# Performance work log

Measured on AMD Instinct MI355X. Metric: run time of the kernel, lower is better.

Reference implementation:

```python
import jax, jax.numpy as jnp
from jax import lax
import numpy as np

DECAY = 0.5   # LIF membrane leak factor
VTH = 1.0     # firing threshold


def _conv(x, w, stride, pad):
    # x: [B,C,H,W], w: [O,I,kh,kw]
    return lax.conv_general_dilated(
        x, w, (stride, stride), [(pad, pad), (pad, pad)],
        dimension_numbers=('NCHW', 'OIHW', 'NCHW'))


def _convT(x, w, b, stride=2, pad=1):
    # torch ConvTranspose2d(in,out,k,stride,pad): w is [Cin,Cout,k,k]
    k = w.shape[-1]
    wf = jnp.flip(w, (-2, -1)).transpose(1, 0, 2, 3)  # -> [Cout,Cin,k,k]
    y = lax.conv_general_dilated(
        x, wf, (1, 1), [(k - 1 - pad, k - 1 - pad)] * 2,
        lhs_dilation=(stride, stride),
        dimension_numbers=('NCHW', 'OIHW', 'NCHW'))
    return y + b[None, :, None, None]


def setup_inputs() -> dict:
    key = jax.random.key(0)
    ks = jax.random.split(key, 8)
    T, B = 16, 32
    x_seq = (jax.random.uniform(ks[0], (T, B, 1, 100, 368)) < 0.1).astype(jnp.float32)

    def p(k, shape, fan_in):
        return jax.random.normal(k, shape, jnp.float32) * (1.0 / np.sqrt(fan_in))

    return {
        'x_seq': x_seq,
        'w1': p(ks[1], (16, 1, 5, 5), 25),
        'w2': p(ks[2], (32, 16, 3, 3), 16 * 9),
        'wd': p(ks[3], (64, 32, 3, 3), 32 * 9),
        'bd': jnp.zeros((64,), jnp.float32),
        'wt1': p(ks[4], (64, 32, 4, 4), 64 * 16),
        'bt1': jnp.zeros((32,), jnp.float32),
        'wt2': p(ks[5], (32, 2, 4, 4), 32 * 16),
        'bt2': jnp.zeros((2,), jnp.float32),
        'actual_batch_size': 32,
    }


def reference(x_seq, w1, w2, wd, bd, wt1, bt1, wt2, bt2, actual_batch_size):
    B = x_seq.shape[1]
    dt = x_seq.dtype
    mem1 = jnp.zeros((B, 16, 50, 184), dt)
    mem2 = jnp.zeros((B, 32, 25, 92), dt)

    def step(carry, x):
        m1, m2 = carry
        # spiking conv layer 1: leaky integrate, fire, hard reset
        m1 = m1 * DECAY + _conv(x, w1, 2, 2)
        s1 = (m1 >= VTH).astype(dt)
        m1 = m1 * (1.0 - s1)
        # spiking conv layer 2 (return_dense -> membrane kept for decoder)
        m2 = m2 * DECAY + _conv(s1, w2, 2, 1)
        s2 = (m2 >= VTH).astype(dt)
        m2 = m2 * (1.0 - s2)
        return (m1, m2), None

    (mem1, mem2), _ = lax.scan(step, (mem1, mem2), x_seq)

    # dense CNN decoder on final membrane state
    h = jax.nn.relu(_conv(mem2, wd, 1, 1) + bd[None, :, None, None])   # [B,64,25,92]
    h = jax.nn.relu(_convT(h, wt1, bt1))                               # [B,32,50,184]
    out = jax.nn.softplus(_convT(h, wt2, bt2))                         # [B,2,100,368]
    inv_tau_c_pred = out[:, 0:1]
    alpha_pred = out[:, 1:2]
    return inv_tau_c_pred, alpha_pred
```

## Files before the change

kernel.cpp:

```cpp
#include <hip/hip_runtime.h>
#include <hip/hip_bf16.h>
#include <cstddef>


#define T_STEPS 16
#define NB 32
#define H0 100
#define W0 368
#define C1 16
#define H1 50
#define W1 184
#define C2 32
#define H2 25
#define W2 92
#define CD 64
#define WPR 6
#define SITES2 2300
#define SITES1 9200

using f32x16 = __attribute__((ext_vector_type(16))) float;
using f32x4  = __attribute__((ext_vector_type(4))) float;
using s16x8  = __attribute__((ext_vector_type(8))) short;

__device__ inline unsigned short f2bf(float f) {
    union { float f; unsigned int u; } v; v.f = f;
    unsigned int r = v.u + 0x7fffu + ((v.u >> 16) & 1u);
    return (unsigned short)(r >> 16);
}
__device__ inline float bf2f(unsigned short u) {
    union { unsigned int u; float f; } v; v.u = ((unsigned int)u) << 16;
    return v.f;
}
__device__ inline unsigned int pk2(float a, float b) {
    return (unsigned int)f2bf(a) | ((unsigned int)f2bf(b) << 16);
}
__device__ inline s16x8 ld8(const void* p) { return *reinterpret_cast<const s16x8*>(p); }

__global__ __launch_bounds__(256) void k_pack(const float* __restrict__ x,
                                              unsigned long long* __restrict__ xb) {
    long long gid = (long long)blockIdx.x * blockDim.x + threadIdx.x;
    long long widx = gid >> 6;
    int lane = (int)(gid & 63);
    const long long NWORDS = (long long)T_STEPS * NB * H0 * WPR;
    if (widx >= NWORDS) return;
    int wcol = (int)(widx % WPR);
    long long rowid = widx / WPR;
    int y = (int)(rowid % H0);
    long long tb = rowid / H0;
    int col = wcol * 64 + lane;
    float v = 0.f;
    if (col < W0) v = x[(tb * H0 + y) * W0 + col];
    unsigned long long mask = __ballot(v != 0.f);
    if (lane == 0) xb[widx] = mask;
}

__global__ __launch_bounds__(256) void k_snn1(const unsigned long long* __restrict__ xb,
                                              const unsigned short* __restrict__ w1b3,
                                              unsigned short* __restrict__ s1m) {
    __shared__ uint4 lut[256];
    {
        int m = (int)threadIdx.x;
        unsigned int wv[4];
#pragma unroll
        for (int h = 0; h < 4; ++h) {
            unsigned int lo = (m >> (2 * h)) & 1u, hb = (m >> (2 * h + 1)) & 1u;
            wv[h] = (lo ? 0x3F80u : 0u) | (hb ? 0x3F800000u : 0u);
        }
        lut[m] = make_uint4(wv[0], wv[1], wv[2], wv[3]);
    }
    __syncthreads();

    int wave = threadIdx.x >> 6;
    int lane = threadIdx.x & 63;
    int col = lane & 15;
    int hi  = lane >> 4;
    const int NPOS = NB * H1 * W1;
    int base = (blockIdx.x * 4 + wave) * 64;

    int site = base + lane;
    int x1 = site % W1;
    int tq = site / W1;
    int y1 = tq % H1;
    int b  = tq / H1;
    const int iy0 = 2 * y1 - 2;
    const int ix0 = 2 * x1 - 2;
    const int wi = ix0 >> 6;
    const int sh = ix0 & 63;

    s16x8 af0 = ld8((const char*)w1b3 + (size_t)((0 * 16 + col) * 32 + hi * 8) * 2);
    s16x8 af1 = ld8((const char*)w1b3 + (size_t)((1 * 16 + col) * 32 + hi * 8) * 2);
    s16x8 af2 = ld8((const char*)w1b3 + (size_t)((2 * 16 + col) * 32 + hi * 8) * 2);

    f32x4 acc0 = {}, acc1 = {}, acc2 = {}, acc3 = {};

    for (int t = 0; t < T_STEPS; ++t) {
#pragma unroll
        for (int e = 0; e < 4; ++e) {
            acc0[e] *= 0.5f; acc1[e] *= 0.5f; acc2[e] *= 0.5f; acc3[e] *= 0.5f;
        }
        const unsigned long long* xp = xb + ((size_t)(t * NB + b) * H0) * WPR;
        unsigned int bits25 = 0;
#pragma unroll
        for (int ky = 0; ky < 5; ++ky) {
            int iy = iy0 + ky;
            if (iy < 0 || iy >= H0) continue;
            const unsigned long long* row = xp + (size_t)iy * WPR;
            unsigned long long a = (wi >= 0) ? row[wi] : 0ull;
            unsigned long long bw = (wi + 1 < WPR) ? row[wi + 1] : 0ull;
            unsigned long long chunk = a >> sh;
            if (sh) chunk |= (bw << (64 - sh));
            bits25 |= ((unsigned int)chunk & 31u) << (5 * ky);
        }
#pragma unroll
        for (int g = 0; g < 4; ++g) {
            unsigned int sb = __shfl(bits25, g * 16 + col, 64);
            unsigned int byte = (sb >> (hi * 8)) & 0xFFu;
            s16x8 bf = *reinterpret_cast<const s16x8*>(&lut[byte]);
            f32x4& ac = (g == 0) ? acc0 : (g == 1) ? acc1 : (g == 2) ? acc2 : acc3;
            ac = __builtin_amdgcn_mfma_f32_16x16x32_bf16(af0, bf, ac, 0, 0, 0);
            ac = __builtin_amdgcn_mfma_f32_16x16x32_bf16(af1, bf, ac, 0, 0, 0);
            ac = __builtin_amdgcn_mfma_f32_16x16x32_bf16(af2, bf, ac, 0, 0, 0);
        }
#pragma unroll
        for (int g = 0; g < 4; ++g) {
            f32x4& ac = (g == 0) ? acc0 : (g == 1) ? acc1 : (g == 2) ? acc2 : acc3;
            unsigned int nib = 0;
#pragma unroll
            for (int e = 0; e < 4; ++e) {
                float v = ac[e];
                bool s = (v >= 1.0f);
                if (s) nib |= (1u << e);
                ac[e] = s ? 0.f : v;
            }
            unsigned int mk = nib << (hi * 4);
            mk |= __shfl_xor(mk, 16, 64);
            mk |= __shfl_xor(mk, 32, 64);
            if (lane < 16)
                s1m[(size_t)t * NPOS + base + g * 16 + lane] = (unsigned short)mk;
        }
    }
}

__global__ __launch_bounds__(256) void k_snn2(const unsigned short* __restrict__ s1m,
                                              const unsigned short* __restrict__ w2b3,
                                              unsigned short* __restrict__ mem2bf) {
    __shared__ uint4 lut[256];
    {
        int m = (int)threadIdx.x;
        unsigned int wv[4];
#pragma unroll
        for (int h = 0; h < 4; ++h) {
            unsigned int lo = (m >> (2 * h)) & 1u, hb = (m >> (2 * h + 1)) & 1u;
            wv[h] = (lo ? 0x3F80u : 0u) | (hb ? 0x3F800000u : 0u);
        }
        lut[m] = make_uint4(wv[0], wv[1], wv[2], wv[3]);
    }
    __syncthreads();

    int wave = threadIdx.x >> 6;
    int lane = threadIdx.x & 63;
    int col = lane & 31, hi = lane >> 5;
    int gsite = (blockIdx.x * 4 + wave) * 32 + col;
    int b = gsite / SITES2;
    int rest = gsite % SITES2;
    int y2 = rest / W2, x2 = rest % W2;

    int toff[9]; bool tval[9];
#pragma unroll
    for (int ky = 0; ky < 3; ++ky)
#pragma unroll
        for (int kx = 0; kx < 3; ++kx) {
            int iy = 2 * y2 + ky - 1, ix = 2 * x2 + kx - 1;
            tval[ky * 3 + kx] = iy >= 0 && iy < H1 && ix >= 0 && ix < W1;
            toff[ky * 3 + kx] = iy * W1 + ix;
        }

    const char* ab = (const char*)w2b3;
    s16x8 a0[9], a1[9], a2[9];
#pragma unroll
    for (int s = 0; s < 9; ++s) {
        int ko = (s * 16 + hi * 8) * 2;
        a0[s] = ld8(ab + (col * 144) * 2 + ko);
        a1[s] = ld8(ab + ((32 + col) * 144) * 2 + ko);
        a2[s] = ld8(ab + ((64 + col) * 144) * 2 + ko);
    }

    f32x16 acc = {};
    int hsh = hi * 8;

    for (int t = 0; t < T_STEPS; ++t) {
        const unsigned short* spk = s1m + (size_t)t * (NB * H1 * W1) + (size_t)b * (H1 * W1);
        unsigned int msk[9];
#pragma unroll
        for (int i = 0; i < 9; ++i)
            msk[i] = tval[i] ? (unsigned int)spk[toff[i]] : 0u;

#pragma unroll
        for (int e = 0; e < 16; ++e) acc[e] *= 0.5f;

#pragma unroll
        for (int s = 0; s < 9; ++s) {
            unsigned int byte = (msk[s] >> hsh) & 0xFFu;
            s16x8 bf = *reinterpret_cast<const s16x8*>(&lut[byte]);
            acc = __builtin_amdgcn_mfma_f32_32x32x16_bf16(a0[s], bf, acc, 0, 0, 0);
            acc = __builtin_amdgcn_mfma_f32_32x32x16_bf16(a1[s], bf, acc, 0, 0, 0);
            acc = __builtin_amdgcn_mfma_f32_32x32x16_bf16(a2[s], bf, acc, 0, 0, 0);
        }
#pragma unroll
        for (int e = 0; e < 16; ++e) {
            float v = acc[e];
            acc[e] = (v >= 1.0f) ? 0.f : v;
        }
    }

    char* obase = (char*)(mem2bf + (size_t)gsite * C2);
#pragma unroll
    for (int q = 0; q < 4; ++q) {
        int co = 8 * q + 4 * hi;
        uint2 u;
        u.x = pk2(acc[4 * q + 0], acc[4 * q + 1]);
        u.y = pk2(acc[4 * q + 2], acc[4 * q + 3]);
        *(uint2*)(obase + co * 2) = u;
    }
}

__global__ __launch_bounds__(256) void k_repackb(const float* __restrict__ wd,
                                                 const float* __restrict__ wt1,
                                                 const float* __restrict__ wt2,
                                                 const float* __restrict__ w2,
                                                 const float* __restrict__ w1,
                                                 unsigned short* __restrict__ wdb,
                                                 unsigned short* __restrict__ wt1b,
                                                 float* __restrict__ wt2k,
                                                 unsigned short* __restrict__ w2b3,
                                                 unsigned short* __restrict__ w1b3) {
    int gid = blockIdx.x * blockDim.x + threadIdx.x;
    if (gid < 64 * 288) {
        int co = gid / 288, k = gid % 288;
        int tap = k >> 5, ci = k & 31;
        wdb[gid] = f2bf(wd[((size_t)co * C2 + ci) * 9 + tap]);
    } else if (gid < 64 * 288 + 4 * 32 * 256) {
        int j = gid - 64 * 288;
        int par = j >> 13, co = (j >> 8) & 31, k = j & 255;
        int tap = k >> 6, ci = k & 63;
        int ty = tap >> 1, tx = tap & 1;
        int ry = par >> 1, rx = par & 1;
        int ky = ry ? (ty ? 0 : 2) : (ty ? 3 : 1);
        int kx = rx ? (tx ? 0 : 2) : (tx ? 3 : 1);
        wt1b[j] = f2bf(wt1[(((size_t)ci * 32 + co) * 4 + ky) * 4 + kx]);
    } else if (gid < 64 * 288 + 4 * 32 * 256 + 1024) {
        int j = gid - (64 * 288 + 4 * 32 * 256);
        int par = j >> 8, tap = (j >> 6) & 3, ci = (j >> 1) & 31, co = j & 1;
        int ty = tap >> 1, tx = tap & 1;
        int ry = par >> 1, rx = par & 1;
        int ky = ry ? (ty ? 0 : 2) : (ty ? 3 : 1);
        int kx = rx ? (tx ? 0 : 2) : (tx ? 3 : 1);
        wt2k[j] = wt2[(((size_t)ci * 2 + co) * 4 + ky) * 4 + kx];
    } else if (gid < 64 * 288 + 4 * 32 * 256 + 1024 + 3 * 32 * 144) {
        int j = gid - (64 * 288 + 4 * 32 * 256 + 1024);
        int p = j / 4608, rem = j % 4608;
        int co = rem / 144, k = rem % 144;
        int tap = k / 16, ci = k % 16;
        float w = w2[((size_t)co * C1 + ci) * 9 + tap];
        unsigned short b0 = f2bf(w);
        float r1 = w - bf2f(b0);
        unsigned short b1 = f2bf(r1);
        float r2 = r1 - bf2f(b1);
        unsigned short b2 = f2bf(r2);
        w2b3[j] = (p == 0) ? b0 : (p == 1) ? b1 : b2;
    } else if (gid < 64 * 288 + 4 * 32 * 256 + 1024 + 3 * 32 * 144 + 3 * 16 * 32) {
        int j = gid - (64 * 288 + 4 * 32 * 256 + 1024 + 3 * 32 * 144);
        int p = j / 512, rem = j % 512;
        int co = rem / 32, k = rem % 32;
        float w = (k < 25) ? w1[co * 25 + k] : 0.f;
        unsigned short b0 = f2bf(w);
        float r1 = w - bf2f(b0);
        unsigned short b1 = f2bf(r1);
        float r2 = r1 - bf2f(b1);
        unsigned short b2 = f2bf(r2);
        w1b3[j] = (p == 0) ? b0 : (p == 1) ? b1 : b2;
    }
}

__global__ __launch_bounds__(256) void k_convd(const unsigned short* __restrict__ mem2bf,
                                               const unsigned short* __restrict__ wdb,
                                               const float* __restrict__ bd,
                                               unsigned short* __restrict__ h1bf) {
    int wave = threadIdx.x >> 6;
    int lane = threadIdx.x & 63;
    int col = lane & 31, hi = lane >> 5;
    int b = blockIdx.z;
    int n0 = (blockIdx.x * 4 + wave) * 32;
    int site = n0 + col;
    bool sval = site < SITES2;
    int sc = sval ? site : 0;
    int yy = sc / W2, xx = sc % W2;

    const char* ibase = (const char*)(mem2bf + (size_t)b * SITES2 * C2);
    int toff[9];
    bool tval[9];
#pragma unroll
    for (int ky = 0; ky < 3; ++ky)
#pragma unroll
        for (int kx = 0; kx < 3; ++kx) {
            int iy = yy + ky - 1, ix = xx + kx - 1;
            bool v = sval && iy >= 0 && iy < H2 && ix >= 0 && ix < W2;
            tval[ky * 3 + kx] = v;
            toff[ky * 3 + kx] = (iy * W2 + ix) * (C2 * 2);
        }

    const char* abase = (const char*)wdb;
    f32x16 acc0 = {}, acc1 = {};
    const s16x8 zero = {0, 0, 0, 0, 0, 0, 0, 0};
#pragma unroll
    for (int s = 0; s < 18; ++s) {
        int tap = s >> 1;
        int boff = (s & 1) * 32 + hi * 16;
        s16x8 bf = tval[tap] ? ld8(ibase + toff[tap] + boff) : zero;
        s16x8 a0 = ld8(abase + col * 576 + s * 32 + hi * 16);
        s16x8 a1 = ld8(abase + (col + 32) * 576 + s * 32 + hi * 16);
        acc0 = __builtin_amdgcn_mfma_f32_32x32x16_bf16(a0, bf, acc0, 0, 0, 0);
        acc1 = __builtin_amdgcn_mfma_f32_32x32x16_bf16(a1, bf, acc1, 0, 0, 0);
    }
    if (!sval) return;
    char* obase = (char*)(h1bf + ((size_t)b * SITES2 + site) * CD);
#pragma unroll
    for (int t = 0; t < 2; ++t) {
        const f32x16& ac = t ? acc1 : acc0;
#pragma unroll
        for (int q = 0; q < 4; ++q) {
            int co = t * 32 + 8 * q + 4 * hi;
            float v0 = fmaxf(ac[4 * q + 0] + bd[co + 0], 0.f);
            float v1 = fmaxf(ac[4 * q + 1] + bd[co + 1], 0.f);
            float v2 = fmaxf(ac[4 * q + 2] + bd[co + 2], 0.f);
            float v3 = fmaxf(ac[4 * q + 3] + bd[co + 3], 0.f);
            uint2 u; u.x = pk2(v0, v1); u.y = pk2(v2, v3);
            *(uint2*)(obase + co * 2) = u;
        }
    }
}

__global__ __launch_bounds__(256) void k_convt1(const unsigned short* __restrict__ h1bf,
                                                const unsigned short* __restrict__ wt1b,
                                                const float* __restrict__ bt1,
                                                unsigned short* __restrict__ h2bf) {
    int wave = threadIdx.x >> 6;
    int lane = threadIdx.x & 63;
    int col = lane & 31, hi = lane >> 5;
    int par = blockIdx.y;
    int ry = par >> 1, rx = par & 1;
    int b = blockIdx.z;
    int n0 = (blockIdx.x * 4 + wave) * 64;

    const char* ibase = (const char*)(h1bf + (size_t)b * SITES2 * CD);
    int toff[2][4];
    bool tval[2][4];
    int mm[2], nn[2];
    bool sv[2];
#pragma unroll
    for (int j = 0; j < 2; ++j) {
        int site = n0 + j * 32 + col;
        sv[j] = site < SITES2;
        int sc = sv[j] ? site : 0;
        int m = sc / W2, n = sc % W2;
        mm[j] = m; nn[j] = n;
        int iy1 = m + (ry ? 1 : -1);
        int ix1 = n + (rx ? 1 : -1);
        bool y1v = iy1 >= 0 && iy1 < H2;
        bool x1v = ix1 >= 0 && ix1 < W2;
#pragma unroll
        for (int t = 0; t < 4; ++t) {
            int ty = t >> 1, tx = t & 1;
            int iy = ty ? iy1 : m;
            int ix = tx ? ix1 : n;
            tval[j][t] = sv[j] && (ty ? y1v : true) && (tx ? x1v : true);
            toff[j][t] = (iy * W2 + ix) * (CD * 2);
        }
    }

    const char* abase = (const char*)(wt1b + (size_t)par * 32 * 256);
    f32x16 acc0 = {}, acc1 = {};
    const s16x8 zero = {0, 0, 0, 0, 0, 0, 0, 0};
#pragma unroll
    for (int s = 0; s < 16; ++s) {
        int tap = s >> 2;
        int boff = (s & 3) * 32 + hi * 16;
        s16x8 b0 = tval[0][tap] ? ld8(ibase + toff[0][tap] + boff) : zero;
        s16x8 b1 = tval[1][tap] ? ld8(ibase + toff[1][tap] + boff) : zero;
        s16x8 a = ld8(abase + col * 512 + s * 32 + hi * 16);
        acc0 = __builtin_amdgcn_mfma_f32_32x32x16_bf16(a, b0, acc0, 0, 0, 0);
        acc1 = __builtin_amdgcn_mfma_f32_32x32x16_bf16(a, b1, acc1, 0, 0, 0);
    }
#pragma unroll
    for (int j = 0; j < 2; ++j) {
        if (!sv[j]) continue;
        const f32x16& ac = j ? acc1 : acc0;
        int oy = 2 * mm[j] + ry, ox = 2 * nn[j] + rx;
        char* obase = (char*)(h2bf + ((size_t)b * SITES1 + (size_t)oy * W1 + ox) * C2);
#pragma unroll
        for (int q = 0; q < 4; ++q) {
            int co = 8 * q + 4 * hi;
            float v0 = fmaxf(ac[4 * q + 0] + bt1[co + 0], 0.f);
            float v1 = fmaxf(ac[4 * q + 1] + bt1[co + 1], 0.f);
            float v2 = fmaxf(ac[4 * q + 2] + bt1[co + 2], 0.f);
            float v3 = fmaxf(ac[4 * q + 3] + bt1[co + 3], 0.f);
            uint2 u; u.x = pk2(v0, v1); u.y = pk2(v2, v3);
            *(uint2*)(obase + co * 2) = u;
        }
    }
}

__global__ __launch_bounds__(256) void k_convt2(const unsigned short* __restrict__ h2bf,
                                                const float* __restrict__ wt2k,
                                                const float* __restrict__ bt2,
                                                float* __restrict__ out) {
    int i = blockIdx.x * blockDim.x + threadIdx.x;
    if (i >= SITES1) return;
    int par = blockIdx.y;
    int ry = par >> 1, rx = par & 1;
    int b = blockIdx.z;
    int m = i / W1, n = i % W1;
    int iy1 = m + (ry ? 1 : -1);
    int ix1 = n + (rx ? 1 : -1);
    bool y1v = iy1 >= 0 && iy1 < H1;
    bool x1v = ix1 >= 0 && ix1 < W1;

    float a0 = bt2[0], a1 = bt2[1];
    const unsigned short* ib = h2bf + (size_t)b * SITES1 * C2;
#pragma unroll
    for (int t = 0; t < 4; ++t) {
        int ty = t >> 1, tx = t & 1;
        if ((ty && !y1v) || (tx && !x1v)) continue;
        int iy = ty ? iy1 : m;
        int ix = tx ? ix1 : n;
        const unsigned short* p = ib + ((size_t)iy * W1 + ix) * C2;
        const float* w = wt2k + ((size_t)par * 4 + t) * 64;
#pragma unroll
        for (int g = 0; g < 4; ++g) {
            s16x8 v8 = ld8(p + g * 8);
#pragma unroll
            for (int e = 0; e < 8; ++e) {
                float v = bf2f((unsigned short)v8[e]);
                int ci = g * 8 + e;
                a0 += v * w[2 * ci];
                a1 += v * w[2 * ci + 1];
            }
        }
    }
    int oy = 2 * m + ry, ox = 2 * n + rx;
    size_t base_o = (size_t)b * (H0 * W0) + (size_t)oy * W0 + ox;
    out[base_o] = fmaxf(a0, 0.f) + log1pf(expf(-fabsf(a0)));
    out[(size_t)NB * H0 * W0 + base_o] = fmaxf(a1, 0.f) + log1pf(expf(-fabsf(a1)));
}

extern "C" void kernel_launch(void* const* d_in, const int* in_sizes, int n_in,
                              void* d_out, int out_size, void* d_ws, size_t ws_size,
                              hipStream_t stream) {
    const float* x   = (const float*)d_in[0];
    const float* w1  = (const float*)d_in[1];
    const float* w2  = (const float*)d_in[2];
    const float* wd  = (const float*)d_in[3];
    const float* bd  = (const float*)d_in[4];
    const float* wt1 = (const float*)d_in[5];
    const float* bt1 = (const float*)d_in[6];
    const float* wt2 = (const float*)d_in[7];
    const float* bt2 = (const float*)d_in[8];
    float* out = (float*)d_out;

    char* ws = (char*)d_ws;
    unsigned short* s1m    = (unsigned short*)(ws);
    unsigned short* mem2bf = (unsigned short*)(ws + 9420800);
    unsigned short* h1bf   = (unsigned short*)(ws + 14131200);
    unsigned short* h2bf   = (unsigned short*)(ws + 23552000);
    unsigned long long* xb = (unsigned long long*)(ws + 42393600);
    unsigned short* wdb    = (unsigned short*)(ws + 44851200);
    unsigned short* wt1b   = (unsigned short*)(ws + 44888064);
    float* wt2k            = (float*)(ws + 44953600);
    unsigned short* w2b3   = (unsigned short*)(ws + 44957696);
    unsigned short* w1b3   = (unsigned short*)(ws + 44985344);

    {
        int n = 64 * 288 + 4 * 32 * 256 + 1024 + 3 * 32 * 144 + 3 * 16 * 32;
        k_repackb<<<(n + 255) / 256, 256, 0, stream>>>(wd, wt1, wt2, w2, w1,
                                                       wdb, wt1b, wt2k, w2b3, w1b3);
    }
    {
        long long nthreads = (long long)T_STEPS * NB * H0 * WPR * 64;
        int blocks = (int)((nthreads + 255) / 256);
        k_pack<<<blocks, 256, 0, stream>>>(x, xb);
    }
    {
        k_snn1<<<1150, 256, 0, stream>>>(xb, w1b3, s1m);
    }
    {
        k_snn2<<<575, 256, 0, stream>>>(s1m, w2b3, mem2bf);
    }
    {
        dim3 g(18, 1, NB);
        k_convd<<<g, 256, 0, stream>>>(mem2bf, wdb, bd, h1bf);
    }
    {
        dim3 g(9, 4, NB);
        k_convt1<<<g, 256, 0, stream>>>(h1bf, wt1b, bt1, h2bf);
    }
    {
        dim3 g(36, 4, NB);
        k_convt2<<<g, 256, 0, stream>>>(h2bf, wt2k, bt2, out);
    }
}
```

Before: 200.2 us.

## Split 5x5 spike-window extraction into separate kernel and store spikes as byte planes

Moves the per-site 25-bit input window gathering out of the SNN layer-1 time loop into a new fully parallel kernel that writes a bitmask per (t, site). k_snn1 then loads these precomputed masks with a one-step prefetch instead of doing five row reads plus a shuffle each step. Layer-1 spikes are stored as two byte planes per timestep rather than 16-bit words, so k_snn2 indexes the LUT directly without shifting. This adds an extra launch and roughly 19 MB of intermediate mask traffic in exchange for a shorter serial dependency chain in the recurrent kernel.

```diff
diff --git a/kernel.cpp b/kernel.cpp
--- a/kernel.cpp
+++ b/kernel.cpp
@@ -17,6 +17,7 @@
 #define WPR 6
 #define SITES2 2300
 #define SITES1 9200
+#define NPOS1 (NB * H1 * W1)
 
 using f32x16 = __attribute__((ext_vector_type(16))) float;
 using f32x4  = __attribute__((ext_vector_type(4))) float;
@@ -54,30 +55,11 @@
     if (lane == 0) xb[widx] = mask;
 }
 
-__global__ __launch_bounds__(256) void k_snn1(const unsigned long long* __restrict__ xb,
-                                              const unsigned short* __restrict__ w1b3,
-                                              unsigned short* __restrict__ s1m) {
-    __shared__ uint4 lut[256];
-    {
-        int m = (int)threadIdx.x;
-        unsigned int wv[4];
-#pragma unroll
-        for (int h = 0; h < 4; ++h) {
-            unsigned int lo = (m >> (2 * h)) & 1u, hb = (m >> (2 * h + 1)) & 1u;
-            wv[h] = (lo ? 0x3F80u : 0u) | (hb ? 0x3F800000u : 0u);
-        }
-        lut[m] = make_uint4(wv[0], wv[1], wv[2], wv[3]);
-    }
-    __syncthreads();
-
-    int wave = threadIdx.x >> 6;
-    int lane = threadIdx.x & 63;
-    int col = lane & 15;
-    int hi  = lane >> 4;
-    const int NPOS = NB * H1 * W1;
-    int base = (blockIdx.x * 4 + wave) * 64;
-
-    int site = base + lane;
+__global__ __launch_bounds__(256) void k_mask(const unsigned long long* __restrict__ xb,
+                                              unsigned int* __restrict__ bm) {
+    int gid = blockIdx.x * blockDim.x + threadIdx.x;
+    int t = gid / NPOS1;
+    int site = gid - t * NPOS1;
     int x1 = site % W1;
     int tq = site / W1;
     int y1 = tq % H1;
@@ -86,6 +68,43 @@
     const int ix0 = 2 * x1 - 2;
     const int wi = ix0 >> 6;
     const int sh = ix0 & 63;
+    const unsigned long long* xp = xb + ((size_t)(t * NB + b) * H0) * WPR;
+    unsigned int bits25 = 0;
+#pragma unroll
+    for (int ky = 0; ky < 5; ++ky) {
+        int iy = iy0 + ky;
+        if (iy < 0 || iy >= H0) continue;
+        const unsigned long long* row = xp + (size_t)iy * WPR;
+        unsigned long long a = (wi >= 0) ? row[wi] : 0ull;
+        unsigned long long bw = (wi + 1 < WPR) ? row[wi + 1] : 0ull;
+        unsigned long long chunk = a >> sh;
+        if (sh) chunk |= (bw << (64 - sh));
+        bits25 |= ((unsigned int)chunk & 31u) << (5 * ky);
+    }
+    bm[gid] = bits25;
+}
+
+__global__ __launch_bounds__(256) void k_snn1(const unsigned int* __restrict__ bm,
+                                              const unsigned short* __restrict__ w1b3,
+                                              unsigned char* __restrict__ s1b) {
+    __shared__ uint4 lut[256];
+    {
+        int m = (int)threadIdx.x;
+        unsigned int wv[4];
+#pragma unroll
+        for (int h = 0; h < 4; ++h) {
+            unsigned int lo = (m >> (2 * h)) & 1u, hb = (m >> (2 * h + 1)) & 1u;
+            wv[h] = (lo ? 0x3F80u : 0u) | (hb ? 0x3F800000u : 0u);
+        }
+        lut[m] = make_uint4(wv[0], wv[1], wv[2], wv[3]);
+    }
+    __syncthreads();
+
+    int wave = threadIdx.x >> 6;
+    int lane = threadIdx.x & 63;
+    int col = lane & 15;
+    int hi  = lane >> 4;
+    int base = (blockIdx.x * 4 + wave) * 64;
 
     s16x8 af0 = ld8((const char*)w1b3 + (size_t)((0 * 16 + col) * 32 + hi * 8) * 2);
     s16x8 af1 = ld8((const char*)w1b3 + (size_t)((1 * 16 + col) * 32 + hi * 8) * 2);
@@ -93,27 +112,25 @@
 
     f32x4 acc0 = {}, acc1 = {}, acc2 = {}, acc3 = {};
 
+    unsigned int cm0, cm1, cm2, cm3;
+    {
+        const unsigned int* bp = bm + base;
+        cm0 = bp[col]; cm1 = bp[16 + col]; cm2 = bp[32 + col]; cm3 = bp[48 + col];
+    }
+
     for (int t = 0; t < T_STEPS; ++t) {
+        unsigned int nm0 = 0, nm1 = 0, nm2 = 0, nm3 = 0;
+        if (t < T_STEPS - 1) {
+            const unsigned int* bp = bm + (size_t)(t + 1) * NPOS1 + base;
+            nm0 = bp[col]; nm1 = bp[16 + col]; nm2 = bp[32 + col]; nm3 = bp[48 + col];
+        }
 #pragma unroll
         for (int e = 0; e < 4; ++e) {
             acc0[e] *= 0.5f; acc1[e] *= 0.5f; acc2[e] *= 0.5f; acc3[e] *= 0.5f;
         }
-        const unsigned long long* xp = xb + ((size_t)(t * NB + b) * H0) * WPR;
-        unsigned int bits25 = 0;
-#pragma unroll
-        for (int ky = 0; ky < 5; ++ky) {
-            int iy = iy0 + ky;
-            if (iy < 0 || iy >= H0) continue;
-            const unsigned long long* row = xp + (size_t)iy * WPR;
-            unsigned long long a = (wi >= 0) ? row[wi] : 0ull;
-            unsigned long long bw = (wi + 1 < WPR) ? row[wi + 1] : 0ull;
-            unsigned long long chunk = a >> sh;
-            if (sh) chunk |= (bw << (64 - sh));
-            bits25 |= ((unsigned int)chunk & 31u) << (5 * ky);
-        }
 #pragma unroll
         for (int g = 0; g < 4; ++g) {
-            unsigned int sb = __shfl(bits25, g * 16 + col, 64);
+            unsigned int sb = (g == 0) ? cm0 : (g == 1) ? cm1 : (g == 2) ? cm2 : cm3;
             unsigned int byte = (sb >> (hi * 8)) & 0xFFu;
             s16x8 bf = *reinterpret_cast<const s16x8*>(&lut[byte]);
             f32x4& ac = (g == 0) ? acc0 : (g == 1) ? acc1 : (g == 2) ? acc2 : acc3;
@@ -132,16 +149,18 @@
                 if (s) nib |= (1u << e);
                 ac[e] = s ? 0.f : v;
             }
-            unsigned int mk = nib << (hi * 4);
+            unsigned int mk = nib << ((hi & 1) * 4);
             mk |= __shfl_xor(mk, 16, 64);
-            mk |= __shfl_xor(mk, 32, 64);
-            if (lane < 16)
-                s1m[(size_t)t * NPOS + base + g * 16 + lane] = (unsigned short)mk;
-        }
-    }
-}
-
-__global__ __launch_bounds__(256) void k_snn2(const unsigned short* __restrict__ s1m,
+            if (hi == 0)
+                s1b[(size_t)(t * 2 + 0) * NPOS1 + base + g * 16 + col] = (unsigned char)mk;
+            else if (hi == 2)
+                s1b[(size_t)(t * 2 + 1) * NPOS1 + base + g * 16 + col] = (unsigned char)mk;
+        }
+        cm0 = nm0; cm1 = nm1; cm2 = nm2; cm3 = nm3;
+    }
+}
+
+__global__ __launch_bounds__(256) void k_snn2(const unsigned char* __restrict__ s1b,
                                               const unsigned short* __restrict__ w2b3,
                                               unsigned short* __restrict__ mem2bf) {
     __shared__ uint4 lut[256];
@@ -186,10 +205,9 @@
     }
 
     f32x16 acc = {};
-    int hsh = hi * 8;
 
     for (int t = 0; t < T_STEPS; ++t) {
-        const unsigned short* spk = s1m + (size_t)t * (NB * H1 * W1) + (size_t)b * (H1 * W1);
+        const unsigned char* spk = s1b + (size_t)(t * 2 + hi) * NPOS1 + (size_t)b * (H1 * W1);
         unsigned int msk[9];
 #pragma unroll
         for (int i = 0; i < 9; ++i)
@@ -200,8 +218,7 @@
 
 #pragma unroll
         for (int s = 0; s < 9; ++s) {
-            unsigned int byte = (msk[s] >> hsh) & 0xFFu;
-            s16x8 bf = *reinterpret_cast<const s16x8*>(&lut[byte]);
+            s16x8 bf = *reinterpret_cast<const s16x8*>(&lut[msk[s]]);
             acc = __builtin_amdgcn_mfma_f32_32x32x16_bf16(a0[s], bf, acc, 0, 0, 0);
             acc = __builtin_amdgcn_mfma_f32_32x32x16_bf16(a1[s], bf, acc, 0, 0, 0);
             acc = __builtin_amdgcn_mfma_f32_32x32x16_bf16(a2[s], bf, acc, 0, 0, 0);
@@ -468,7 +485,7 @@
     float* out = (float*)d_out;
 
     char* ws = (char*)d_ws;
-    unsigned short* s1m    = (unsigned short*)(ws);
+    unsigned char* s1b     = (unsigned char*)(ws);
     unsigned short* mem2bf = (unsigned short*)(ws + 9420800);
     unsigned short* h1bf   = (unsigned short*)(ws + 14131200);
     unsigned short* h2bf   = (unsigned short*)(ws + 23552000);
@@ -478,6 +495,7 @@
     float* wt2k            = (float*)(ws + 44953600);
     unsigned short* w2b3   = (unsigned short*)(ws + 44957696);
     unsigned short* w1b3   = (unsigned short*)(ws + 44985344);
+    unsigned int* bm       = (unsigned int*)(ws + 44988416);
 
     {
         int n = 64 * 288 + 4 * 32 * 256 + 1024 + 3 * 32 * 144 + 3 * 16 * 32;
@@ -490,10 +508,13 @@
         k_pack<<<blocks, 256, 0, stream>>>(x, xb);
     }
     {
-        k_snn1<<<1150, 256, 0, stream>>>(xb, w1b3, s1m);
-    }
-    {
-        k_snn2<<<575, 256, 0, stream>>>(s1m, w2b3, mem2bf);
+        k_mask<<<18400, 256, 0, stream>>>(xb, bm);
+    }
+    {
+        k_snn1<<<1150, 256, 0, stream>>>(bm, w1b3, s1b);
+    }
+    {
+        k_snn2<<<575, 256, 0, stream>>>(s1b, w2b3, mem2bf);
     }
     {
         dim3 g(18, 1, NB);
```

Result: slower. 210.3 us (+5.1%).
